# Kernel tuning notes

Hardware: AMD Instinct MI355X
Metric: run time of the kernel (lower is better)

## Reference

```python
import jax, jax.numpy as jnp
import numpy as np

IN_CH = 256
OUT_CH = 256
K = 3
STRIDE = 1
PAD = 1
NUM_EMB = 8


def setup_inputs() -> dict:
    key = jax.random.key(0)
    ks = jax.random.split(key, 6)
    B, H, W = 16, 64, 64
    x = jax.random.normal(ks[0], (B, IN_CH, H, W), dtype=jnp.float32)
    kernal_embed = jax.random.normal(ks[1], (NUM_EMB, IN_CH, OUT_CH, K, K), dtype=jnp.float32)
    # 1x1 conv params (stored as a dense [out,in] matrix) + bias
    cls_conv_w = jax.random.normal(ks[2], (IN_CH, IN_CH), dtype=jnp.float32) / np.sqrt(IN_CH)
    cls_conv_b = jax.random.normal(ks[3], (IN_CH,), dtype=jnp.float32) * 0.01
    cls_dense_w = jax.random.normal(ks[4], (NUM_EMB, IN_CH), dtype=jnp.float32) / np.sqrt(IN_CH)
    cls_dense_b = jax.random.normal(ks[5], (NUM_EMB,), dtype=jnp.float32) * 0.01
    return {"x": x, "kernal_embed": kernal_embed, "cls_conv_w": cls_conv_w,
            "cls_conv_b": cls_conv_b, "cls_dense_w": cls_dense_w, "cls_dense_b": cls_dense_b}


def reference(x, kernal_embed, cls_conv_w, cls_conv_b, cls_dense_w, cls_dense_b):
    B, C, H, W = x.shape
    # 1x1 conv -> global avg pool -> dense -> softmax weights over embeddings
    w = jnp.einsum('bchw,dc->bdhw', x, cls_conv_w) + cls_conv_b[None, :, None, None]
    pooled = jnp.mean(w, axis=(2, 3))                       # (B, C)
    logits = pooled @ cls_dense_w.T + cls_dense_b           # (B, E)
    mix = jax.nn.softmax(logits, axis=1)                    # (B, E)
    # Per-sample kernel synthesis: (B, in, out, k, k)
    kern = jnp.einsum('be,eiojk->biojk', mix, kernal_embed)
    # Faithful to torch .view(-1, in, k, k): raw reshape (mixes in/out axes as in original)
    kern = kern.reshape(B, OUT_CH, IN_CH, K, K)
    # Grouped conv with groups=B == per-sample conv via vmap
    def conv1(xi, wi):
        # xi: (C, H, W), wi: (out, in, k, k)
        return jax.lax.conv_general_dilated(
            xi[None], wi, window_strides=(STRIDE, STRIDE),
            padding=[(PAD, PAD), (PAD, PAD)],
            dimension_numbers=('NCHW', 'OIHW', 'NCHW'))[0]
    out = jax.vmap(conv1)(x, kern)                          # (B, out, H, W)
    return out
```

## Files before the change

kernel.cpp:

```cpp
#include <hip/hip_runtime.h>
#include <stdint.h>

#define B_  16
#define C_  256
#define H_  64
#define W_  64
#define P_  4096
#define E_  8
#define HP_ 66

typedef __bf16 bf16x8 __attribute__((ext_vector_type(8)));
typedef float  f32x4  __attribute__((ext_vector_type(4)));

__device__ __forceinline__ unsigned short f2bf(float f) {
    union { float f; unsigned int u; } v; v.f = f;
    unsigned int u = v.u;
    unsigned int r = (u + 0x7fffu + ((u >> 16) & 1u)) >> 16;
    return (unsigned short)r;
}

__device__ __forceinline__ void async_load16(const void* g, void* l) {
    __builtin_amdgcn_global_load_lds(
        (const __attribute__((address_space(1))) void*)g,
        (__attribute__((address_space(3))) void*)l, 16, 0, 0);
}

__global__ void k_xpose(const float* __restrict__ x, unsigned short* __restrict__ Xp,
                        float* __restrict__ xsum) {
    const int bid = blockIdx.x;
    const int b  = bid >> 8;
    const int h  = (bid >> 2) & 63;
    const int cg = bid & 3;
    const int c0 = cg << 6;
    const int tid = threadIdx.x;
    __shared__ float tile[64][65];
    {
        const int ci = tid >> 2, wseg = tid & 3;
        const float* src = x + ((size_t)(b * 256 + c0 + ci) << 12) + (h << 6) + wseg * 16;
        float s = 0.f;
#pragma unroll
        for (int i = 0; i < 4; ++i) {
            float4 v = *(const float4*)(src + i * 4);
            tile[ci][wseg * 16 + i * 4 + 0] = v.x;
            tile[ci][wseg * 16 + i * 4 + 1] = v.y;
            tile[ci][wseg * 16 + i * 4 + 2] = v.z;
            tile[ci][wseg * 16 + i * 4 + 3] = v.w;
            s += v.x + v.y + v.z + v.w;
        }
        s += __shfl_down(s, 1, 64);
        s += __shfl_down(s, 2, 64);
        if ((tid & 3) == 0) atomicAdd(&xsum[b * 256 + c0 + ci], s);
    }
    __syncthreads();
    {
        const int w = tid >> 2, cs = tid & 3;
        unsigned short ov[16] __attribute__((aligned(16)));
#pragma unroll
        for (int k = 0; k < 16; ++k) ov[k] = f2bf(tile[cs * 16 + k][w]);
        unsigned short* dst = Xp + ((size_t)((b * HP_ + h + 1) * HP_ + (w + 1)) << 8) + c0 + cs * 16;
        ((uint4*)dst)[0] = ((const uint4*)ov)[0];
        ((uint4*)dst)[1] = ((const uint4*)ov)[1];
    }
}

__global__ void k_mix(const float* __restrict__ xsum,
                      const float* __restrict__ cw, const float* __restrict__ cb,
                      const float* __restrict__ dw, const float* __restrict__ db,
                      float* __restrict__ mix) {
    const int b = blockIdx.x, tid = threadIdx.x;
    __shared__ float sxm[256];
    __shared__ float spool[256];
    __shared__ float sl[8];
    sxm[tid] = xsum[b * 256 + tid] * (1.0f / P_);
    __syncthreads();
    float a = cb[tid];
    for (int c = 0; c < 256; ++c) a += cw[tid * 256 + c] * sxm[c];
    spool[tid] = a;
    __syncthreads();
    if (tid < 8) {
        float l = db[tid];
        for (int d = 0; d < 256; ++d) l += dw[tid * 256 + d] * spool[d];
        sl[tid] = l;
    }
    __syncthreads();
    if (tid < 8) {
        float m = sl[0];
        for (int e = 1; e < 8; ++e) m = fmaxf(m, sl[e]);
        float den = 0.f;
        for (int e = 0; e < 8; ++e) den += __expf(sl[e] - m);
        mix[b * 8 + tid] = __expf(sl[tid] - m) / den;
    }
}

__global__ void k_mixkern(const float* __restrict__ KE, const float* __restrict__ mix,
                          unsigned short* __restrict__ Wg) {
    const int o    = blockIdx.x >> 1;
    const int half = blockIdx.x & 1;
    const int ic0  = half << 7;
    const int tid  = threadIdx.x;
    __shared__ float s[8][1152];
    __shared__ float smix[128];
    if (tid < 128) smix[tid] = mix[tid];
#pragma unroll
    for (int e = 0; e < 8; ++e) {
        const float* src = KE + (size_t)(e * 256 + o) * 2304 + ic0 * 9;
#pragma unroll
        for (int k = 0; k < 4; ++k) s[e][k * 256 + tid] = src[k * 256 + tid];
        if (tid < 128) s[e][1024 + tid] = src[1024 + tid];
    }
    __syncthreads();
    const int icl = tid & 127;
    const int b0  = (tid >> 7) << 3;
#pragma unroll
    for (int t = 0; t < 9; ++t) {
        float v[8];
#pragma unroll
        for (int e = 0; e < 8; ++e) v[e] = s[e][icl * 9 + t];
#pragma unroll
        for (int bb = 0; bb < 8; ++bb) {
            const int b = b0 + bb;
            float acc = 0.f;
#pragma unroll
            for (int e = 0; e < 8; ++e) acc += smix[b * 8 + e] * v[e];
            Wg[((size_t)(b * 256 + o) * 9 + t) * 256 + ic0 + icl] = f2bf(acc);
        }
    }
}

__global__ void k_border(unsigned short* __restrict__ Xp) {
    const int gid = blockIdx.x * 256 + threadIdx.x;
    const int pix = gid >> 5;
    const int chunk = gid & 31;
    const int b = pix / 260;
    const int j = pix - b * 260;
    int h, w;
    if (j < 66)       { h = 0;  w = j; }
    else if (j < 132) { h = 65; w = j - 66; }
    else { int jj = j - 132; h = 1 + (jj & 63); w = (jj < 64) ? 0 : 65; }
    const uint4 z = {0u, 0u, 0u, 0u};
    *(uint4*)(Xp + ((size_t)((b * HP_ + h) * HP_ + w) << 8) + chunk * 8) = z;
}

__global__ __launch_bounds__(256) void k_gemm(const unsigned short* __restrict__ Wg,
                                              const unsigned short* __restrict__ Xp,
                                              float* __restrict__ out) {
    __shared__ __align__(16) unsigned short lA[128 * 64];
    __shared__ __align__(16) unsigned short lB[128 * 64];
    const int tid = threadIdx.x;
    const int bid = blockIdx.x;
    const int xcd = bid & 7;
    const int g   = bid >> 3;
    const int b   = xcd + ((g >> 6) << 3);
    const int rem = g & 63;
    const int ot  = rem & 1;
    const int rp  = rem >> 1;
    const int o0  = ot << 7;
    const int h0  = rp << 1;

    const int wid  = tid >> 6;
    const int lane = tid & 63;
    const int wm   = wid >> 1;
    const int wn   = wid & 1;
    const int ql   = lane & 15;
    const int quad = lane >> 4;
    const int sw   = ql & 7;

    const int srow = tid >> 3;
    const int sseg = tid & 7;
    const int csrc = sseg ^ (srow & 7);

    f32x4 acc[4][4];
#pragma unroll
    for (int i = 0; i < 4; ++i)
#pragma unroll
        for (int j = 0; j < 4; ++j) acc[i][j] = (f32x4)0.0f;

    char* lAb = (char*)lA;
    char* lBb = (char*)lB;
    const size_t abase = (size_t)(b * 256 + o0 + srow) * 9 * 256 + csrc * 8;

    for (int t = 0; t < 9; ++t) {
        const int kh = t / 3;
        const int kw = t - kh * 3;
        for (int kc = 0; kc < 4; ++kc) {
#pragma unroll
            for (int j = 0; j < 4; ++j) {
                const unsigned short* ga = Wg + abase + (size_t)j * 32 * 9 * 256
                                           + (size_t)t * 256 + kc * 64;
                async_load16(ga, lAb + tid * 16 + j * 4096);
            }
#pragma unroll
            for (int j = 0; j < 4; ++j) {
                const int pix = srow + 32 * j;
                const int pr  = pix >> 6;
                const int w   = pix & 63;
                const unsigned short* gb = Xp
                    + ((size_t)((b * HP_ + h0 + pr + kh) * HP_ + (w + kw)) << 8)
                    + kc * 64 + csrc * 8;
                async_load16(gb, lBb + tid * 16 + j * 4096);
            }
            __syncthreads();
#pragma unroll
            for (int kk = 0; kk < 2; ++kk) {
                bf16x8 af[4], bv[4];
#pragma unroll
                for (int mi = 0; mi < 4; ++mi)
                    af[mi] = *(const bf16x8*)(lAb + (wm * 64 + mi * 16 + ql) * 128
                                              + ((((kk << 2) | quad) ^ sw) << 4));
#pragma unroll
                for (int ni = 0; ni < 4; ++ni)
                    bv[ni] = *(const bf16x8*)(lBb + (wn * 64 + ni * 16 + ql) * 128
                                              + ((((kk << 2) | quad) ^ sw) << 4));
#pragma unroll
                for (int mi = 0; mi < 4; ++mi)
#pragma unroll
                    for (int ni = 0; ni < 4; ++ni)
                        acc[mi][ni] = __builtin_amdgcn_mfma_f32_16x16x32_bf16(
                            af[mi], bv[ni], acc[mi][ni], 0, 0, 0);
            }
            __syncthreads();
        }
    }

    const int h = h0 + wn;
#pragma unroll
    for (int mi = 0; mi < 4; ++mi) {
        const int o = o0 + wm * 64 + mi * 16 + quad * 4;
#pragma unroll
        for (int ni = 0; ni < 4; ++ni) {
            const int w = ni * 16 + ql;
            float* po = out + ((size_t)(b * 256 + o) << 12) + (h << 6) + w;
#pragma unroll
            for (int r = 0; r < 4; ++r) po[(size_t)r << 12] = acc[mi][ni][r];
        }
    }
}

extern "C" void kernel_launch(void* const* d_in, const int* in_sizes, int n_in,
                              void* d_out, int out_size, void* d_ws, size_t ws_size,
                              hipStream_t stream) {
    const float* x  = (const float*)d_in[0];
    const float* KE = (const float*)d_in[1];
    const float* cw = (const float*)d_in[2];
    const float* cb = (const float*)d_in[3];
    const float* dw = (const float*)d_in[4];
    const float* db = (const float*)d_in[5];
    float* out = (float*)d_out;

    char* ws = (char*)d_ws;
    float* xsum           = (float*)(ws + 0);
    float* mix            = (float*)(ws + 16384);
    unsigned short* Wg    = (unsigned short*)(ws + 32768);
    unsigned short* Xp    = (unsigned short*)(ws + 32768 + 18874368);

    hipMemsetAsync(xsum, 0, B_ * C_ * sizeof(float), stream);
    k_xpose  <<<dim3(B_ * H_ * 4),    dim3(256), 0, stream>>>(x, Xp, xsum);
    k_border <<<dim3(520),            dim3(256), 0, stream>>>(Xp);
    k_mix    <<<dim3(B_),             dim3(256), 0, stream>>>(xsum, cw, cb, dw, db, mix);
    k_mixkern<<<dim3(C_ * 2),         dim3(256), 0, stream>>>(KE, mix, Wg);
    k_gemm   <<<dim3(B_ * 2 * 32),    dim3(256), 0, stream>>>(Wg, Xp, out);
}
```

Before: 264.3 us.

## Fold border zeroing into transpose kernel, vectorize mix and kernel-mix loads

Adds the padding-border zeroing as extra blocks of the transpose kernel, removing one launch. Rewrites the tiny mix kernel so each wavefront computes dot products with coalesced float4 loads and shuffle reductions, replacing strided per-thread row loops. Switches the kernel-embedding staging in k_mixkern to float4 global loads. Together these aim to cut launch overhead and uncoalesced accesses in the small preprocessing kernels, while the big GEMM is unchanged.

```diff
diff --git a/kernel.cpp b/kernel.cpp
--- a/kernel.cpp
+++ b/kernel.cpp
@@ -27,12 +27,26 @@
 
 __global__ void k_xpose(const float* __restrict__ x, unsigned short* __restrict__ Xp,
                         float* __restrict__ xsum) {
-    const int bid = blockIdx.x;
-    const int b  = bid >> 8;
-    const int h  = (bid >> 2) & 63;
-    const int cg = bid & 3;
+    const int bid0 = blockIdx.x;
+    const int tid = threadIdx.x;
+    if (bid0 >= B_ * H_ * 4) {
+        const int gid = (bid0 - B_ * H_ * 4) * 256 + tid;
+        const int pix = gid >> 5;
+        const int chunk = gid & 31;
+        const int b = pix / 260;
+        const int j = pix - b * 260;
+        int h, w;
+        if (j < 66)       { h = 0;  w = j; }
+        else if (j < 132) { h = 65; w = j - 66; }
+        else { int jj = j - 132; h = 1 + (jj & 63); w = (jj < 64) ? 0 : 65; }
+        const uint4 z = {0u, 0u, 0u, 0u};
+        *(uint4*)(Xp + ((size_t)((b * HP_ + h) * HP_ + w) << 8) + chunk * 8) = z;
+        return;
+    }
+    const int b  = bid0 >> 8;
+    const int h  = (bid0 >> 2) & 63;
+    const int cg = bid0 & 3;
     const int c0 = cg << 6;
-    const int tid = threadIdx.x;
     __shared__ float tile[64][65];
     {
         const int ci = tid >> 2, wseg = tid & 3;
@@ -68,19 +82,30 @@
                       const float* __restrict__ dw, const float* __restrict__ db,
                       float* __restrict__ mix) {
     const int b = blockIdx.x, tid = threadIdx.x;
-    __shared__ float sxm[256];
-    __shared__ float spool[256];
+    const int wave = tid >> 6, lane = tid & 63;
+    __shared__ __align__(16) float sxm[256];
+    __shared__ __align__(16) float spool[256];
     __shared__ float sl[8];
     sxm[tid] = xsum[b * 256 + tid] * (1.0f / P_);
     __syncthreads();
-    float a = cb[tid];
-    for (int c = 0; c < 256; ++c) a += cw[tid * 256 + c] * sxm[c];
-    spool[tid] = a;
-    __syncthreads();
-    if (tid < 8) {
-        float l = db[tid];
-        for (int d = 0; d < 256; ++d) l += dw[tid * 256 + d] * spool[d];
-        sl[tid] = l;
+    const float4 xm4 = *(const float4*)(sxm + lane * 4);
+#pragma unroll 4
+    for (int i = 0; i < 64; ++i) {
+        const int d = i * 4 + wave;
+        const float4 w4 = *(const float4*)(cw + (size_t)d * 256 + lane * 4);
+        float p = w4.x * xm4.x + w4.y * xm4.y + w4.z * xm4.z + w4.w * xm4.w;
+        for (int off = 32; off; off >>= 1) p += __shfl_down(p, off, 64);
+        if (lane == 0) spool[d] = p + cb[d];
+    }
+    __syncthreads();
+    const float4 pp4 = *(const float4*)(spool + lane * 4);
+#pragma unroll
+    for (int i = 0; i < 2; ++i) {
+        const int e = i * 4 + wave;
+        const float4 w4 = *(const float4*)(dw + (size_t)e * 256 + lane * 4);
+        float p = w4.x * pp4.x + w4.y * pp4.y + w4.z * pp4.z + w4.w * pp4.w;
+        for (int off = 32; off; off >>= 1) p += __shfl_down(p, off, 64);
+        if (lane == 0) sl[e] = p + db[e];
     }
     __syncthreads();
     if (tid < 8) {
@@ -98,15 +123,15 @@
     const int half = blockIdx.x & 1;
     const int ic0  = half << 7;
     const int tid  = threadIdx.x;
-    __shared__ float s[8][1152];
+    __shared__ __align__(16) float s[8][1152];
     __shared__ float smix[128];
     if (tid < 128) smix[tid] = mix[tid];
 #pragma unroll
     for (int e = 0; e < 8; ++e) {
-        const float* src = KE + (size_t)(e * 256 + o) * 2304 + ic0 * 9;
-#pragma unroll
-        for (int k = 0; k < 4; ++k) s[e][k * 256 + tid] = src[k * 256 + tid];
-        if (tid < 128) s[e][1024 + tid] = src[1024 + tid];
+        const float4* src4 = (const float4*)(KE + (size_t)(e * 256 + o) * 2304 + ic0 * 9);
+        float4* d4 = (float4*)&s[e][0];
+        d4[tid] = src4[tid];
+        if (tid < 32) d4[256 + tid] = src4[256 + tid];
     }
     __syncthreads();
     const int icl = tid & 127;
@@ -125,20 +150,6 @@
             Wg[((size_t)(b * 256 + o) * 9 + t) * 256 + ic0 + icl] = f2bf(acc);
         }
     }
-}
-
-__global__ void k_border(unsigned short* __restrict__ Xp) {
-    const int gid = blockIdx.x * 256 + threadIdx.x;
-    const int pix = gid >> 5;
-    const int chunk = gid & 31;
-    const int b = pix / 260;
-    const int j = pix - b * 260;
-    int h, w;
-    if (j < 66)       { h = 0;  w = j; }
-    else if (j < 132) { h = 65; w = j - 66; }
-    else { int jj = j - 132; h = 1 + (jj & 63); w = (jj < 64) ? 0 : 65; }
-    const uint4 z = {0u, 0u, 0u, 0u};
-    *(uint4*)(Xp + ((size_t)((b * HP_ + h) * HP_ + w) << 8) + chunk * 8) = z;
 }
 
 __global__ __launch_bounds__(256) void k_gemm(const unsigned short* __restrict__ Wg,
@@ -254,9 +265,8 @@
     unsigned short* Xp    = (unsigned short*)(ws + 32768 + 18874368);
 
     hipMemsetAsync(xsum, 0, B_ * C_ * sizeof(float), stream);
-    k_xpose  <<<dim3(B_ * H_ * 4),    dim3(256), 0, stream>>>(x, Xp, xsum);
-    k_border <<<dim3(520),            dim3(256), 0, stream>>>(Xp);
-    k_mix    <<<dim3(B_),             dim3(256), 0, stream>>>(xsum, cw, cb, dw, db, mix);
-    k_mixkern<<<dim3(C_ * 2),         dim3(256), 0, stream>>>(KE, mix, Wg);
-    k_gemm   <<<dim3(B_ * 2 * 32),    dim3(256), 0, stream>>>(Wg, Xp, out);
-}
+    k_xpose  <<<dim3(B_ * H_ * 4 + 520), dim3(256), 0, stream>>>(x, Xp, xsum);
+    k_mix    <<<dim3(B_),                dim3(256), 0, stream>>>(xsum, cw, cb, dw, db, mix);
+    k_mixkern<<<dim3(C_ * 2),            dim3(256), 0, stream>>>(KE, mix, Wg);
+    k_gemm   <<<dim3(B_ * 2 * 32),       dim3(256), 0, stream>>>(Wg, Xp, out);
+}
```

Result: slower. 291.7 us (+10.4%).
